# Kernel optimization log

Hardware: AMD Instinct MI355X
Metric: run time of the kernel (lower is better)

## Reference

```python
import jax, jax.numpy as jnp
import numpy as np

B, L, D, NLAYERS, KCONV = 8, 2048, 1024, 3, 4


def setup_inputs() -> dict:
    key = jax.random.key(0)
    ks = jax.random.split(key, 8)
    inp = {
        "x": jax.random.normal(ks[0], (B, L, D), jnp.float32),
        "conv_w": jax.random.normal(ks[1], (NLAYERS, D, KCONV), jnp.float32) * 0.02,
        "conv_b": jnp.zeros((NLAYERS, D), jnp.float32),
        "wr_w": jax.random.normal(ks[2], (NLAYERS, D, D), jnp.float32) * (1.0 / np.sqrt(D)),
        "wr_b": jnp.zeros((NLAYERS, D), jnp.float32),
        "wi_w": jax.random.normal(ks[3], (NLAYERS, D, D), jnp.float32) * (1.0 / np.sqrt(D)),
        "wi_b": jnp.zeros((NLAYERS, D), jnp.float32),
        "log_a": 3.0 + 0.1 * jax.random.normal(ks[4], (NLAYERS, D), jnp.float32),
        "wo_w": jax.random.normal(ks[5], (NLAYERS, D, D), jnp.float32) * (1.0 / np.sqrt(D)),
        "norm_w": jnp.ones((NLAYERS, D), jnp.float32),
        "norm_out_w": jnp.ones((D,), jnp.float32),
    }
    return inp


def _rmsnorm(x, w, eps=1e-6):
    return x * w * jax.lax.rsqrt(jnp.mean(x * x, axis=-1, keepdims=True) + eps)


def _parallel_scan(a, b):
    # h_t = a_t * h_{t-1} + b_t  via log-space prefix scan (h0 = 0)
    a32 = a.astype(jnp.float32)
    b32 = b.astype(jnp.float32)
    log_A = jnp.cumsum(jnp.log(jnp.maximum(a32, 1e-7)), axis=1)
    log_A = jnp.maximum(log_A, -80.0)  # a<=1 so log_A<=0 already
    A = jnp.exp(log_A)
    h = A * jnp.cumsum(b32 * jnp.exp(-log_A), axis=1)
    return h.astype(a.dtype)


def _rglru_layer(x, cw, cb, wrw, wrb, wiw, wib, la, wow, nw):
    # causal depthwise conv1d, kernel 4, left pad 3
    Lx = x.shape[1]
    xp = jnp.pad(x, ((0, 0), (KCONV - 1, 0), (0, 0)))
    x_conv = cb + sum(xp[:, k:k + Lx, :] * cw[:, k] for k in range(KCONV))
    r_t = jax.nn.sigmoid(x_conv @ wrw.T + wrb)
    i_t = jax.nn.sigmoid(x_conv @ wiw.T + wib)
    a_base = jax.nn.sigmoid(la.astype(jnp.float32)).astype(x.dtype)
    a_t = a_base ** (8.0 * r_t)
    b_t = jnp.sqrt(jnp.clip(1.0 - a_t * a_t, 1e-6, None)) * (i_t * x_conv)
    h = _parallel_scan(a_t, b_t)
    return _rmsnorm(h @ wow.T, nw)


def reference(x, conv_w, conv_b, wr_w, wr_b, wi_w, wi_b, log_a, wo_w, norm_w, norm_out_w):
    h = x
    for l in range(NLAYERS):
        h = _rglru_layer(h, conv_w[l], conv_b[l], wr_w[l], wr_b[l],
                         wi_w[l], wi_b[l], log_a[l], wo_w[l], norm_w[l])
    return _rmsnorm(h, norm_out_w)
```

## Files before the change

### kernel.cpp

```cpp
#include <hip/hip_runtime.h>
#include <type_traits>

#define BDIM 8
#define LDIM 2048
#define DDIM 1024
#define NL 3
#define K4 4
#define MDIM (BDIM * LDIM)
#define BK32 32
#define NT32 (DDIM / BK32)

typedef __bf16 bf16x8 __attribute__((ext_vector_type(8)));
typedef __bf16 bf16x4 __attribute__((ext_vector_type(4)));
typedef float f32x4 __attribute__((ext_vector_type(4)));
typedef const __attribute__((address_space(1))) void gvoid_t;
typedef __attribute__((address_space(3))) void svoid_t;

__device__ __forceinline__ void load16(const void* g, void* lds_uniform) {
    __builtin_amdgcn_global_load_lds((gvoid_t*)g, (svoid_t*)lds_uniform, 16, 0, 0);
}

#define SBAR()                                  \
    do {                                        \
        asm volatile("" ::: "memory");          \
        __builtin_amdgcn_s_barrier();           \
        asm volatile("" ::: "memory");          \
    } while (0)
#define WAITV(N) asm volatile("s_waitcnt vmcnt(" #N ")" ::: "memory")

__global__ void cvt_bf16(const float* __restrict__ s, __bf16* __restrict__ d, int n) {
    int i = blockIdx.x * 256 + threadIdx.x;
    if (i < n) d[i] = (__bf16)s[i];
}

__global__ __launch_bounds__(256) void cvt_interleave(const float* __restrict__ wr,
                                                      const float* __restrict__ wi,
                                                      __bf16* __restrict__ w2, int n) {
    int i = blockIdx.x * 256 + threadIdx.x;
    if (i >= n) return;
    int k = i & (DDIM - 1);
    int ld = i >> 10;
    int l = ld >> 10;
    int d = ld & (DDIM - 1);
    size_t base = ((size_t)l * 2 * DDIM + 2 * d) * DDIM + k;
    w2[base] = (__bf16)wr[i];
    w2[base + DDIM] = (__bf16)wi[i];
}

template <typename T>
__global__ __launch_bounds__(256) void conv_kernel(const T* __restrict__ X,
                                                   const float* __restrict__ cw,
                                                   const float* __restrict__ cb,
                                                   __bf16* __restrict__ XC) {
    int idx = blockIdx.x * 256 + threadIdx.x;
    int d = (idx & (DDIM / 4 - 1)) << 2;
    int t = (idx >> 8) & (LDIM - 1);
    int b = idx >> 19;
    float wv[4][4];
    *(float4*)wv[0] = ((const float4*)cw)[d + 0];
    *(float4*)wv[1] = ((const float4*)cw)[d + 1];
    *(float4*)wv[2] = ((const float4*)cw)[d + 2];
    *(float4*)wv[3] = ((const float4*)cw)[d + 3];
    float4 cbv = *(const float4*)(cb + d);
    float acc[4] = {cbv.x, cbv.y, cbv.z, cbv.w};
#pragma unroll
    for (int k = 0; k < K4; k++) {
        int tt = t + k - (K4 - 1);
        if (tt >= 0) {
            size_t off = ((size_t)(b * LDIM + tt) << 10) + d;
            float xv[4];
            if constexpr (std::is_same<T, float>::value) {
                float4 v = *(const float4*)(X + off);
                xv[0] = v.x; xv[1] = v.y; xv[2] = v.z; xv[3] = v.w;
            } else {
                bf16x4 v = *(const bf16x4*)(X + off);
                xv[0] = (float)v.x; xv[1] = (float)v.y; xv[2] = (float)v.z; xv[3] = (float)v.w;
            }
#pragma unroll
            for (int j = 0; j < 4; j++) acc[j] += xv[j] * wv[j][k];
        }
    }
    bf16x4 o;
    o.x = (__bf16)acc[0]; o.y = (__bf16)acc[1]; o.z = (__bf16)acc[2]; o.w = (__bf16)acc[3];
    *(bf16x4*)(XC + ((size_t)(b * LDIM + t) << 10) + d) = o;
}

__global__ __launch_bounds__(512, 2) void gate_gemm(
    const __bf16* __restrict__ A, const __bf16* __restrict__ W2,
    const float* __restrict__ wrb, const float* __restrict__ wib,
    const float* __restrict__ la,
    __bf16* __restrict__ LOGA, __bf16* __restrict__ BB) {
    __shared__ __attribute__((aligned(16))) __bf16 sm[4][2][8192];
    int tid = threadIdx.x;
    int wave = tid >> 6, lane = tid & 63;
    int wm = wave >> 2, wn = wave & 3;
    int fr = lane & 15, quad = lane >> 4;

    int nx = gridDim.x;
    int bid = blockIdx.y * nx + blockIdx.x;
    int cpx = (nx * gridDim.y) >> 3;
    int sw = (bid & 7) * cpx + (bid >> 3);
    int bm0 = (sw / nx) * 256;
    int bn0 = (sw % nx) * 256;

    const __bf16* Ag = A + (size_t)bm0 * DDIM;
    const __bf16* Bg = W2 + (size_t)bn0 * DDIM;

    f32x4 acc[8][4];
    f32x4 zero = {0.f, 0.f, 0.f, 0.f};
#pragma unroll
    for (int i = 0; i < 8; i++)
#pragma unroll
        for (int j = 0; j < 4; j++) acc[i][j] = zero;

    auto STAGE = [&](int buf, int ko) {
#pragma unroll
        for (int j = 0; j < 2; j++) {
            int ci = j * 512 + tid;
            int r = ci >> 2;
            int g = (ci & 3) ^ ((r >> 1) & 3);
            size_t go = (size_t)r * DDIM + ko + g * 8;
            int lb = j * 4096 + wave * 512;
            load16(Ag + go, &sm[buf][0][lb]);
            load16(Bg + go, &sm[buf][1][lb]);
        }
    };

    STAGE(0, 0);
    STAGE(1, BK32);
    STAGE(2, 2 * BK32);
    for (int t4 = 0; t4 < NT32; t4 += 4) {
#pragma unroll
        for (int tt = 0; tt < 4; tt++) {
            int t = t4 + tt;
            if (t + 2 < NT32) { WAITV(8); }
            else if (t + 1 < NT32) { WAITV(4); }
            else { WAITV(0); }
            SBAR();
            if (t + 3 < NT32) STAGE((tt + 3) & 3, (t + 3) * BK32);
            const __bf16* Ac = &sm[tt][0][0];
            const __bf16* Bc = &sm[tt][1][0];
            bf16x8 bfm[4];
#pragma unroll
            for (int ni = 0; ni < 4; ni++) {
                int row = wn * 64 + ni * 16 + fr;
                bfm[ni] = *(const bf16x8*)(Bc + row * 32 + ((quad ^ ((row >> 1) & 3)) << 3));
            }
#pragma unroll
            for (int mh = 0; mh < 2; mh++) {
                bf16x8 af[4];
#pragma unroll
                for (int mi = 0; mi < 4; mi++) {
                    int row = wm * 128 + (mh * 4 + mi) * 16 + fr;
                    af[mi] = *(const bf16x8*)(Ac + row * 32 + ((quad ^ ((row >> 1) & 3)) << 3));
                }
                __builtin_amdgcn_s_setprio(1);
#pragma unroll
                for (int ni = 0; ni < 4; ni++)
#pragma unroll
                    for (int mi = 0; mi < 4; mi++)
                        acc[mh * 4 + mi][ni] = __builtin_amdgcn_mfma_f32_16x16x32_bf16(
                            af[mi], bfm[ni], acc[mh * 4 + mi][ni], 0, 0, 0);
                __builtin_amdgcn_s_setprio(0);
            }
        }
    }

    float* Lt = (float*)&sm[0][0][0];
    int colg = (tid & 31) * 8;
    int d0 = (bn0 >> 1) + (colg >> 1);
    float rb[4], ibv[4], lnab[4];
    {
        float4 r4 = *(const float4*)(wrb + d0);
        float4 i4 = *(const float4*)(wib + d0);
        float4 l4 = *(const float4*)(la + d0);
        float lav[4] = {l4.x, l4.y, l4.z, l4.w};
        rb[0] = r4.x; rb[1] = r4.y; rb[2] = r4.z; rb[3] = r4.w;
        ibv[0] = i4.x; ibv[1] = i4.y; ibv[2] = i4.z; ibv[3] = i4.w;
#pragma unroll
        for (int j = 0; j < 4; j++) lnab[j] = __logf(1.f / (1.f + __expf(-lav[j])));
    }
#pragma unroll
    for (int mi = 0; mi < 8; mi++) {
        __syncthreads();
#pragma unroll
        for (int ni = 0; ni < 4; ni++) {
            int col = wn * 64 + ni * 16 + fr;
#pragma unroll
            for (int reg = 0; reg < 4; reg++)
                Lt[(wm * 16 + quad * 4 + reg) * 260 + col] = acc[mi][ni][reg];
        }
        __syncthreads();
#pragma unroll
        for (int hf = 0; hf < 2; hf++) {
            int r = (tid >> 5) + hf * 16;
            int m = bm0 + (r >> 4) * 128 + mi * 16 + (r & 15);
            float vv[8];
            *(f32x4*)&vv[0] = *(const f32x4*)&Lt[r * 260 + colg];
            *(f32x4*)&vv[4] = *(const f32x4*)&Lt[r * 260 + colg + 4];
            bf16x4 xcv = *(const bf16x4*)(A + (size_t)m * DDIM + d0);
            bf16x4 og, ob;
#pragma unroll
            for (int j = 0; j < 4; j++) {
                float rv = 1.f / (1.f + __expf(-(vv[2 * j] + rb[j])));
                float iv = 1.f / (1.f + __expf(-(vv[2 * j + 1] + ibv[j])));
                float lga = 8.f * rv * lnab[j];
                float a = __expf(lga);
                float bt = sqrtf(fmaxf(1.f - a * a, 1e-6f)) * (iv * (float)xcv[j]);
                og[j] = (__bf16)lga;
                ob[j] = (__bf16)bt;
            }
            *(bf16x4*)(LOGA + (size_t)m * DDIM + d0) = og;
            *(bf16x4*)(BB + (size_t)m * DDIM + d0) = ob;
        }
    }
}

__global__ __launch_bounds__(512, 2) void out_gemm(
    const __bf16* __restrict__ A, const __bf16* __restrict__ Wo, __bf16* __restrict__ HW) {
    __shared__ __attribute__((aligned(16))) __bf16 sm[4][2][8192];
    int tid = threadIdx.x;
    int wave = tid >> 6, lane = tid & 63;
    int wm = wave >> 2, wn = wave & 3;
    int fr = lane & 15, quad = lane >> 4;

    int nx = gridDim.x;
    int bid = blockIdx.y * nx + blockIdx.x;
    int cpx = (nx * gridDim.y) >> 3;
    int sw = (bid & 7) * cpx + (bid >> 3);
    int bm0 = (sw / nx) * 256;
    int bn0 = (sw % nx) * 256;

    const __bf16* Ag = A + (size_t)bm0 * DDIM;
    const __bf16* Bg = Wo + (size_t)bn0 * DDIM;

    f32x4 acc[8][4];
    f32x4 zero = {0.f, 0.f, 0.f, 0.f};
#pragma unroll
    for (int i = 0; i < 8; i++)
#pragma unroll
        for (int j = 0; j < 4; j++) acc[i][j] = zero;

    auto STAGE = [&](int buf, int ko) {
#pragma unroll
        for (int j = 0; j < 2; j++) {
            int ci = j * 512 + tid;
            int r = ci >> 2;
            int g = (ci & 3) ^ ((r >> 1) & 3);
            size_t go = (size_t)r * DDIM + ko + g * 8;
            int lb = j * 4096 + wave * 512;
            load16(Ag + go, &sm[buf][0][lb]);
            load16(Bg + go, &sm[buf][1][lb]);
        }
    };

    STAGE(0, 0);
    STAGE(1, BK32);
    STAGE(2, 2 * BK32);
    for (int t4 = 0; t4 < NT32; t4 += 4) {
#pragma unroll
        for (int tt = 0; tt < 4; tt++) {
            int t = t4 + tt;
            if (t + 2 < NT32) { WAITV(8); }
            else if (t + 1 < NT32) { WAITV(4); }
            else { WAITV(0); }
            SBAR();
            if (t + 3 < NT32) STAGE((tt + 3) & 3, (t + 3) * BK32);
            const __bf16* Ac = &sm[tt][0][0];
            const __bf16* Bc = &sm[tt][1][0];
            bf16x8 bfm[4];
#pragma unroll
            for (int ni = 0; ni < 4; ni++) {
                int row = wn * 64 + ni * 16 + fr;
                bfm[ni] = *(const bf16x8*)(Bc + row * 32 + ((quad ^ ((row >> 1) & 3)) << 3));
            }
#pragma unroll
            for (int mh = 0; mh < 2; mh++) {
                bf16x8 af[4];
#pragma unroll
                for (int mi = 0; mi < 4; mi++) {
                    int row = wm * 128 + (mh * 4 + mi) * 16 + fr;
                    af[mi] = *(const bf16x8*)(Ac + row * 32 + ((quad ^ ((row >> 1) & 3)) << 3));
                }
                __builtin_amdgcn_s_setprio(1);
#pragma unroll
                for (int ni = 0; ni < 4; ni++)
#pragma unroll
                    for (int mi = 0; mi < 4; mi++)
                        acc[mh * 4 + mi][ni] = __builtin_amdgcn_mfma_f32_16x16x32_bf16(
                            af[mi], bfm[ni], acc[mh * 4 + mi][ni], 0, 0, 0);
                __builtin_amdgcn_s_setprio(0);
            }
        }
    }

    float* Lt = (float*)&sm[0][0][0];
    int colg = (tid & 31) * 8;
    int n0 = bn0 + colg;
#pragma unroll
    for (int mi = 0; mi < 8; mi++) {
        __syncthreads();
#pragma unroll
        for (int ni = 0; ni < 4; ni++) {
            int col = wn * 64 + ni * 16 + fr;
#pragma unroll
            for (int reg = 0; reg < 4; reg++)
                Lt[(wm * 16 + quad * 4 + reg) * 260 + col] = acc[mi][ni][reg];
        }
        __syncthreads();
#pragma unroll
        for (int hf = 0; hf < 2; hf++) {
            int r = (tid >> 5) + hf * 16;
            int m = bm0 + (r >> 4) * 128 + mi * 16 + (r & 15);
            float vv[8];
            *(f32x4*)&vv[0] = *(const f32x4*)&Lt[r * 260 + colg];
            *(f32x4*)&vv[4] = *(const f32x4*)&Lt[r * 260 + colg + 4];
            bf16x8 o;
#pragma unroll
            for (int j = 0; j < 8; j++) o[j] = (__bf16)vv[j];
            *(bf16x8*)(HW + (size_t)m * DDIM + n0) = o;
        }
    }
}

#define SC_T (LDIM / 8)
__global__ __launch_bounds__(256) void scan_kernel(const __bf16* __restrict__ LOGA,
                                                   const __bf16* __restrict__ BB,
                                                   __bf16* __restrict__ H) {
    int b = blockIdx.y;
    int dl = threadIdx.x & 31;
    int d = blockIdx.x * 32 + dl;
    int c = threadIdx.x >> 5;
    size_t base = ((size_t)b * LDIM + (size_t)c * SC_T) * DDIM + d;
    const __bf16* pga = LOGA + base;
    const __bf16* pbb = BB + base;
    __bf16* pH = H + base;

    float S = 0.f;
#pragma unroll 8
    for (int t = 0; t < SC_T; t++) S += (float)pga[(size_t)t * DDIM];
    __shared__ float sS[8][32];
    sS[c][dl] = S;
    __syncthreads();
    float L0 = 0.f;
    for (int cc = 0; cc < c; cc++) L0 += sS[cc][dl];

    float Lr = L0, lcp = fmaxf(L0, -80.f), hB = 0.f;
#pragma unroll 4
    for (int t = 0; t < SC_T; t++) {
        float lga = (float)pga[(size_t)t * DDIM];
        Lr += lga;
        float lc = fmaxf(Lr, -80.f);
        hB = __expf(lc - lcp) * hB + (float)pbb[(size_t)t * DDIM];
        lcp = lc;
    }
    float Ac = __expf(fmaxf(Lr, -80.f) - fmaxf(L0, -80.f));
    __shared__ float sA[8][32], sB[8][32];
    sA[c][dl] = Ac;
    sB[c][dl] = hB;
    __syncthreads();
    float hin = 0.f;
    for (int cc = 0; cc < c; cc++) hin = sA[cc][dl] * hin + sB[cc][dl];

    Lr = L0;
    lcp = fmaxf(L0, -80.f);
    float h = hin;
#pragma unroll 4
    for (int t = 0; t < SC_T; t++) {
        float lga = (float)pga[(size_t)t * DDIM];
        Lr += lga;
        float lc = fmaxf(Lr, -80.f);
        h = __expf(lc - lcp) * h + (float)pbb[(size_t)t * DDIM];
        lcp = lc;
        pH[(size_t)t * DDIM] = (__bf16)h;
    }
}

template <typename TI, typename TO>
__global__ __launch_bounds__(256) void rmsnorm_kernel(const TI* __restrict__ X,
                                                      const float* __restrict__ w,
                                                      TO* __restrict__ Y) {
    int row = blockIdx.x;
    int tid = threadIdx.x;
    size_t off = (size_t)row * DDIM + tid * 4;
    float v[4];
    if constexpr (std::is_same<TI, float>::value) {
        float4 t = *(const float4*)(X + off);
        v[0] = t.x; v[1] = t.y; v[2] = t.z; v[3] = t.w;
    } else {
        bf16x4 t = *(const bf16x4*)(X + off);
        v[0] = (float)t.x; v[1] = (float)t.y; v[2] = (float)t.z; v[3] = (float)t.w;
    }
    float s = v[0] * v[0] + v[1] * v[1] + v[2] * v[2] + v[3] * v[3];
#pragma unroll
    for (int o = 32; o > 0; o >>= 1) s += __shfl_down(s, o);
    __shared__ float sw[4];
    if ((tid & 63) == 0) sw[tid >> 6] = s;
    __syncthreads();
    float tot = sw[0] + sw[1] + sw[2] + sw[3];
    float scale = rsqrtf(tot * (1.f / (float)DDIM) + 1e-6f);
    float4 wv = ((const float4*)w)[tid];
    float o0 = v[0] * wv.x * scale, o1 = v[1] * wv.y * scale;
    float o2 = v[2] * wv.z * scale, o3 = v[3] * wv.w * scale;
    if constexpr (std::is_same<TO, float>::value) {
        float4 o = {o0, o1, o2, o3};
        *(float4*)(Y + off) = o;
    } else {
        bf16x4 o;
        o.x = (__bf16)o0; o.y = (__bf16)o1; o.z = (__bf16)o2; o.w = (__bf16)o3;
        *(bf16x4*)(Y + off) = o;
    }
}

extern "C" void kernel_launch(void* const* d_in, const int* in_sizes, int n_in,
                              void* d_out, int out_size, void* d_ws, size_t ws_size,
                              hipStream_t stream) {
    const float* x = (const float*)d_in[0];
    const float* conv_w = (const float*)d_in[1];
    const float* conv_b = (const float*)d_in[2];
    const float* wr_w = (const float*)d_in[3];
    const float* wr_b = (const float*)d_in[4];
    const float* wi_w = (const float*)d_in[5];
    const float* wi_b = (const float*)d_in[6];
    const float* log_a = (const float*)d_in[7];
    const float* wo_w = (const float*)d_in[8];
    const float* norm_w = (const float*)d_in[9];
    const float* norm_out_w = (const float*)d_in[10];

    const size_t W2SZ = (size_t)NL * 2 * DDIM * DDIM;
    const size_t WOSZ = (size_t)NL * DDIM * DDIM;
    const size_t MD = (size_t)MDIM * DDIM;
    __bf16* w2 = (__bf16*)d_ws;
    __bf16* wo16 = w2 + W2SZ;
    __bf16* XC = wo16 + WOSZ;
    __bf16* LGA = XC + MD;
    __bf16* BBf = LGA + MD;
    __bf16* Hb = BBf + MD;
    __bf16* HWb = Hb + MD;
    __bf16* PNb = HWb + MD;

    int nw = (int)WOSZ;
    cvt_interleave<<<(nw + 255) / 256, 256, 0, stream>>>(wr_w, wi_w, w2, nw);
    cvt_bf16<<<(nw + 255) / 256, 256, 0, stream>>>(wo_w, wo16, nw);

    for (int l = 0; l < NL; l++) {
        if (l == 0)
            conv_kernel<float><<<(MDIM * (DDIM / 4)) / 256, 256, 0, stream>>>(
                x, conv_w, conv_b, XC);
        else
            conv_kernel<__bf16><<<(MDIM * (DDIM / 4)) / 256, 256, 0, stream>>>(
                PNb, conv_w + (size_t)l * DDIM * K4, conv_b + (size_t)l * DDIM, XC);
        gate_gemm<<<dim3(2 * DDIM / 256, MDIM / 256), 512, 0, stream>>>(
            XC, w2 + (size_t)l * 2 * DDIM * DDIM,
            wr_b + (size_t)l * DDIM, wi_b + (size_t)l * DDIM, log_a + (size_t)l * DDIM,
            LGA, BBf);
        scan_kernel<<<dim3(DDIM / 32, BDIM), 256, 0, stream>>>(LGA, BBf, Hb);
        out_gemm<<<dim3(DDIM / 256, MDIM / 256), 512, 0, stream>>>(
            Hb, wo16 + (size_t)l * DDIM * DDIM, HWb);
        rmsnorm_kernel<__bf16, __bf16><<<MDIM, 256, 0, stream>>>(
            HWb, norm_w + (size_t)l * DDIM, PNb);
    }
    rmsnorm_kernel<__bf16, float><<<MDIM, 256, 0, stream>>>(PNb, norm_out_w, (float*)d_out);
}
```

Measured before the change: 1.004 ms.

## Shrink GEMM tiles to 128x128 single-buffered, widen scan chunks, fuse final norms

Both GEMMs go from 256x256 tiles with 512 threads and a 4-stage async LDS pipeline to 128x128 tiles with 256 threads, BK=64 and one LDS buffer with a barrier before and after each load. The scan kernel splits the sequence into 32 chunks per block (1024 threads) instead of 8, for more parallelism. The last layer's rmsnorm and the output rmsnorm are fused into one kernel, saving a launch and one pass over memory. Smaller tiles add occupancy and grid size, but they lower per-tile reuse and drop the load/compute overlap, which may hurt GEMM throughput.

Result: faster. 891.3 us (-11.3%).

```diff
diff --git a/kernel.cpp b/kernel.cpp
--- a/kernel.cpp
+++ b/kernel.cpp
@@ -7,8 +7,6 @@
 #define NL 3
 #define K4 4
 #define MDIM (BDIM * LDIM)
-#define BK32 32
-#define NT32 (DDIM / BK32)
 
 typedef __bf16 bf16x8 __attribute__((ext_vector_type(8)));
 typedef __bf16 bf16x4 __attribute__((ext_vector_type(4)));
@@ -19,14 +17,6 @@
 __device__ __forceinline__ void load16(const void* g, void* lds_uniform) {
     __builtin_amdgcn_global_load_lds((gvoid_t*)g, (svoid_t*)lds_uniform, 16, 0, 0);
 }
-
-#define SBAR()                                  \
-    do {                                        \
-        asm volatile("" ::: "memory");          \
-        __builtin_amdgcn_s_barrier();           \
-        asm volatile("" ::: "memory");          \
-    } while (0)
-#define WAITV(N) asm volatile("s_waitcnt vmcnt(" #N ")" ::: "memory")
 
 __global__ void cvt_bf16(const float* __restrict__ s, __bf16* __restrict__ d, int n) {
     int i = blockIdx.x * 256 + threadIdx.x;
@@ -85,89 +75,80 @@
     *(bf16x4*)(XC + ((size_t)(b * LDIM + t) << 10) + d) = o;
 }
 
-__global__ __launch_bounds__(512, 2) void gate_gemm(
+__global__ __launch_bounds__(256, 3) void gate_gemm(
     const __bf16* __restrict__ A, const __bf16* __restrict__ W2,
     const float* __restrict__ wrb, const float* __restrict__ wib,
     const float* __restrict__ la,
     __bf16* __restrict__ LOGA, __bf16* __restrict__ BB) {
-    __shared__ __attribute__((aligned(16))) __bf16 sm[4][2][8192];
+    __shared__ __attribute__((aligned(16))) __bf16 sm[16384];
     int tid = threadIdx.x;
     int wave = tid >> 6, lane = tid & 63;
-    int wm = wave >> 2, wn = wave & 3;
+    int wm = wave >> 1, wn = wave & 1;
     int fr = lane & 15, quad = lane >> 4;
 
     int nx = gridDim.x;
     int bid = blockIdx.y * nx + blockIdx.x;
     int cpx = (nx * gridDim.y) >> 3;
     int sw = (bid & 7) * cpx + (bid >> 3);
-    int bm0 = (sw / nx) * 256;
-    int bn0 = (sw % nx) * 256;
+    int bm0 = (sw / nx) * 128;
+    int bn0 = (sw % nx) * 128;
 
     const __bf16* Ag = A + (size_t)bm0 * DDIM;
     const __bf16* Bg = W2 + (size_t)bn0 * DDIM;
 
-    f32x4 acc[8][4];
+    f32x4 acc[4][4];
     f32x4 zero = {0.f, 0.f, 0.f, 0.f};
 #pragma unroll
-    for (int i = 0; i < 8; i++)
+    for (int i = 0; i < 4; i++)
 #pragma unroll
         for (int j = 0; j < 4; j++) acc[i][j] = zero;
 
-    auto STAGE = [&](int buf, int ko) {
-#pragma unroll
-        for (int j = 0; j < 2; j++) {
-            int ci = j * 512 + tid;
-            int r = ci >> 2;
-            int g = (ci & 3) ^ ((r >> 1) & 3);
-            size_t go = (size_t)r * DDIM + ko + g * 8;
-            int lb = j * 4096 + wave * 512;
-            load16(Ag + go, &sm[buf][0][lb]);
-            load16(Bg + go, &sm[buf][1][lb]);
-        }
-    };
-
-    STAGE(0, 0);
-    STAGE(1, BK32);
-    STAGE(2, 2 * BK32);
-    for (int t4 = 0; t4 < NT32; t4 += 4) {
-#pragma unroll
-        for (int tt = 0; tt < 4; tt++) {
-            int t = t4 + tt;
-            if (t + 2 < NT32) { WAITV(8); }
-            else if (t + 1 < NT32) { WAITV(4); }
-            else { WAITV(0); }
-            SBAR();
-            if (t + 3 < NT32) STAGE((tt + 3) & 3, (t + 3) * BK32);
-            const __bf16* Ac = &sm[tt][0][0];
-            const __bf16* Bc = &sm[tt][1][0];
-            bf16x8 bfm[4];
+    const __bf16* gAs[4];
+    const __bf16* gBs[4];
+    int ub[4];
+#pragma unroll
+    for (int j = 0; j < 4; j++) {
+        int ci = j * 256 + tid;
+        int r = ci >> 3, sc = ci & 7;
+        int g = sc ^ (r & 7);
+        gAs[j] = Ag + (size_t)r * DDIM + g * 8;
+        gBs[j] = Bg + (size_t)r * DDIM + g * 8;
+        ub[j] = (j * 256 + wave * 64) * 8;
+    }
+
+    for (int ko = 0; ko < DDIM; ko += 64) {
+        if (ko) __syncthreads();
+#pragma unroll
+        for (int j = 0; j < 4; j++) {
+            load16(gAs[j] + ko, sm + ub[j]);
+            load16(gBs[j] + ko, sm + 8192 + ub[j]);
+        }
+        __syncthreads();
+#pragma unroll
+        for (int kw = 0; kw < 2; kw++) {
+            bf16x8 af[4], bf[4];
+#pragma unroll
+            for (int mi = 0; mi < 4; mi++) {
+                int row = wm * 64 + mi * 16 + fr;
+                af[mi] = *(const bf16x8*)(sm + row * 64 + (((kw * 4 + quad) ^ (row & 7)) << 3));
+            }
 #pragma unroll
             for (int ni = 0; ni < 4; ni++) {
                 int row = wn * 64 + ni * 16 + fr;
-                bfm[ni] = *(const bf16x8*)(Bc + row * 32 + ((quad ^ ((row >> 1) & 3)) << 3));
-            }
-#pragma unroll
-            for (int mh = 0; mh < 2; mh++) {
-                bf16x8 af[4];
-#pragma unroll
-                for (int mi = 0; mi < 4; mi++) {
-                    int row = wm * 128 + (mh * 4 + mi) * 16 + fr;
-                    af[mi] = *(const bf16x8*)(Ac + row * 32 + ((quad ^ ((row >> 1) & 3)) << 3));
-                }
-                __builtin_amdgcn_s_setprio(1);
-#pragma unroll
-                for (int ni = 0; ni < 4; ni++)
-#pragma unroll
-                    for (int mi = 0; mi < 4; mi++)
-                        acc[mh * 4 + mi][ni] = __builtin_amdgcn_mfma_f32_16x16x32_bf16(
-                            af[mi], bfm[ni], acc[mh * 4 + mi][ni], 0, 0, 0);
-                __builtin_amdgcn_s_setprio(0);
-            }
-        }
-    }
-
-    float* Lt = (float*)&sm[0][0][0];
-    int colg = (tid & 31) * 8;
+                bf[ni] = *(const bf16x8*)(sm + 8192 + row * 64 + (((kw * 4 + quad) ^ (row & 7)) << 3));
+            }
+#pragma unroll
+            for (int ni = 0; ni < 4; ni++)
+#pragma unroll
+                for (int mi = 0; mi < 4; mi++)
+                    acc[mi][ni] = __builtin_amdgcn_mfma_f32_16x16x32_bf16(
+                        af[mi], bf[ni], acc[mi][ni], 0, 0, 0);
+        }
+    }
+
+    float* Lt = (float*)&sm[0];
+    int wrow = (wave >> 1) * 16, wcol = (wave & 1) * 64;
+    int colg = (tid & 15) * 8;
     int d0 = (bn0 >> 1) + (colg >> 1);
     float rb[4], ibv[4], lnab[4];
     {
@@ -181,23 +162,23 @@
         for (int j = 0; j < 4; j++) lnab[j] = __logf(1.f / (1.f + __expf(-lav[j])));
     }
 #pragma unroll
-    for (int mi = 0; mi < 8; mi++) {
+    for (int mi = 0; mi < 4; mi++) {
         __syncthreads();
 #pragma unroll
         for (int ni = 0; ni < 4; ni++) {
-            int col = wn * 64 + ni * 16 + fr;
+            int col = wcol + ni * 16 + fr;
 #pragma unroll
             for (int reg = 0; reg < 4; reg++)
-                Lt[(wm * 16 + quad * 4 + reg) * 260 + col] = acc[mi][ni][reg];
+                Lt[(wrow + quad * 4 + reg) * 132 + col] = acc[mi][ni][reg];
         }
         __syncthreads();
 #pragma unroll
         for (int hf = 0; hf < 2; hf++) {
-            int r = (tid >> 5) + hf * 16;
-            int m = bm0 + (r >> 4) * 128 + mi * 16 + (r & 15);
+            int lrow = (tid >> 4) + hf * 16;
+            int m = bm0 + (lrow >> 4) * 64 + mi * 16 + (lrow & 15);
             float vv[8];
-            *(f32x4*)&vv[0] = *(const f32x4*)&Lt[r * 260 + colg];
-            *(f32x4*)&vv[4] = *(const f32x4*)&Lt[r * 260 + colg + 4];
+            *(f32x4*)&vv[0] = *(const f32x4*)&Lt[lrow * 132 + colg];
+            *(f32x4*)&vv[4] = *(const f32x4*)&Lt[lrow * 132 + colg + 4];
             bf16x4 xcv = *(const bf16x4*)(A + (size_t)m * DDIM + d0);
             bf16x4 og, ob;
 #pragma unroll
@@ -216,105 +197,96 @@
     }
 }
 
-__global__ __launch_bounds__(512, 2) void out_gemm(
+__global__ __launch_bounds__(256, 3) void out_gemm(
     const __bf16* __restrict__ A, const __bf16* __restrict__ Wo, __bf16* __restrict__ HW) {
-    __shared__ __attribute__((aligned(16))) __bf16 sm[4][2][8192];
+    __shared__ __attribute__((aligned(16))) __bf16 sm[16384];
     int tid = threadIdx.x;
     int wave = tid >> 6, lane = tid & 63;
-    int wm = wave >> 2, wn = wave & 3;
+    int wm = wave >> 1, wn = wave & 1;
     int fr = lane & 15, quad = lane >> 4;
 
     int nx = gridDim.x;
     int bid = blockIdx.y * nx + blockIdx.x;
     int cpx = (nx * gridDim.y) >> 3;
     int sw = (bid & 7) * cpx + (bid >> 3);
-    int bm0 = (sw / nx) * 256;
-    int bn0 = (sw % nx) * 256;
+    int bm0 = (sw / nx) * 128;
+    int bn0 = (sw % nx) * 128;
 
     const __bf16* Ag = A + (size_t)bm0 * DDIM;
     const __bf16* Bg = Wo + (size_t)bn0 * DDIM;
 
-    f32x4 acc[8][4];
+    f32x4 acc[4][4];
     f32x4 zero = {0.f, 0.f, 0.f, 0.f};
 #pragma unroll
-    for (int i = 0; i < 8; i++)
+    for (int i = 0; i < 4; i++)
 #pragma unroll
         for (int j = 0; j < 4; j++) acc[i][j] = zero;
 
-    auto STAGE = [&](int buf, int ko) {
-#pragma unroll
-        for (int j = 0; j < 2; j++) {
-            int ci = j * 512 + tid;
-            int r = ci >> 2;
-            int g = (ci & 3) ^ ((r >> 1) & 3);
-            size_t go = (size_t)r * DDIM + ko + g * 8;
-            int lb = j * 4096 + wave * 512;
-            load16(Ag + go, &sm[buf][0][lb]);
-            load16(Bg + go, &sm[buf][1][lb]);
-        }
-    };
-
-    STAGE(0, 0);
-    STAGE(1, BK32);
-    STAGE(2, 2 * BK32);
-    for (int t4 = 0; t4 < NT32; t4 += 4) {
-#pragma unroll
-        for (int tt = 0; tt < 4; tt++) {
-            int t = t4 + tt;
-            if (t + 2 < NT32) { WAITV(8); }
-            else if (t + 1 < NT32) { WAITV(4); }
-            else { WAITV(0); }
-            SBAR();
-            if (t + 3 < NT32) STAGE((tt + 3) & 3, (t + 3) * BK32);
-            const __bf16* Ac = &sm[tt][0][0];
-            const __bf16* Bc = &sm[tt][1][0];
-            bf16x8 bfm[4];
+    const __bf16* gAs[4];
+    const __bf16* gBs[4];
+    int ub[4];
+#pragma unroll
+    for (int j = 0; j < 4; j++) {
+        int ci = j * 256 + tid;
+        int r = ci >> 3, sc = ci & 7;
+        int g = sc ^ (r & 7);
+        gAs[j] = Ag + (size_t)r * DDIM + g * 8;
+        gBs[j] = Bg + (size_t)r * DDIM + g * 8;
+        ub[j] = (j * 256 + wave * 64) * 8;
+    }
+
+    for (int ko = 0; ko < DDIM; ko += 64) {
+        if (ko) __syncthreads();
+#pragma unroll
+        for (int j = 0; j < 4; j++) {
+            load16(gAs[j] + ko, sm + ub[j]);
+            load16(gBs[j] + ko, sm + 8192 + ub[j]);
+        }
+        __syncthreads();
+#pragma unroll
+        for (int kw = 0; kw < 2; kw++) {
+            bf16x8 af[4], bf[4];
+#pragma unroll
+            for (int mi = 0; mi < 4; mi++) {
+                int row = wm * 64 + mi * 16 + fr;
+                af[mi] = *(const bf16x8*)(sm + row * 64 + (((kw * 4 + quad) ^ (row & 7)) << 3));
+            }
 #pragma unroll
             for (int ni = 0; ni < 4; ni++) {
                 int row = wn * 64 + ni * 16 + fr;
-                bfm[ni] = *(const bf16x8*)(Bc + row * 32 + ((quad ^ ((row >> 1) & 3)) << 3));
-            }
-#pragma unroll
-            for (int mh = 0; mh < 2; mh++) {
-                bf16x8 af[4];
-#pragma unroll
-                for (int mi = 0; mi < 4; mi++) {
-                    int row = wm * 128 + (mh * 4 + mi) * 16 + fr;
-                    af[mi] = *(const bf16x8*)(Ac + row * 32 + ((quad ^ ((row >> 1) & 3)) << 3));
-                }
-                __builtin_amdgcn_s_setprio(1);
-#pragma unroll
-                for (int ni = 0; ni < 4; ni++)
-#pragma unroll
-                    for (int mi = 0; mi < 4; mi++)
-                        acc[mh * 4 + mi][ni] = __builtin_amdgcn_mfma_f32_16x16x32_bf16(
-                            af[mi], bfm[ni], acc[mh * 4 + mi][ni], 0, 0, 0);
-                __builtin_amdgcn_s_setprio(0);
-            }
-        }
-    }
-
-    float* Lt = (float*)&sm[0][0][0];
-    int colg = (tid & 31) * 8;
+                bf[ni] = *(const bf16x8*)(sm + 8192 + row * 64 + (((kw * 4 + quad) ^ (row & 7)) << 3));
+            }
+#pragma unroll
+            for (int ni = 0; ni < 4; ni++)
+#pragma unroll
+                for (int mi = 0; mi < 4; mi++)
+                    acc[mi][ni] = __builtin_amdgcn_mfma_f32_16x16x32_bf16(
+                        af[mi], bf[ni], acc[mi][ni], 0, 0, 0);
+        }
+    }
+
+    float* Lt = (float*)&sm[0];
+    int wrow = (wave >> 1) * 16, wcol = (wave & 1) * 64;
+    int colg = (tid & 15) * 8;
     int n0 = bn0 + colg;
 #pragma unroll
-    for (int mi = 0; mi < 8; mi++) {
+    for (int mi = 0; mi < 4; mi++) {
         __syncthreads();
 #pragma unroll
         for (int ni = 0; ni < 4; ni++) {
-            int col = wn * 64 + ni * 16 + fr;
+            int col = wcol + ni * 16 + fr;
 #pragma unroll
             for (int reg = 0; reg < 4; reg++)
-                Lt[(wm * 16 + quad * 4 + reg) * 260 + col] = acc[mi][ni][reg];
+                Lt[(wrow + quad * 4 + reg) * 132 + col] = acc[mi][ni][reg];
         }
         __syncthreads();
 #pragma unroll
         for (int hf = 0; hf < 2; hf++) {
-            int r = (tid >> 5) + hf * 16;
-            int m = bm0 + (r >> 4) * 128 + mi * 16 + (r & 15);
+            int lrow = (tid >> 4) + hf * 16;
+            int m = bm0 + (lrow >> 4) * 64 + mi * 16 + (lrow & 15);
             float vv[8];
-            *(f32x4*)&vv[0] = *(const f32x4*)&Lt[r * 260 + colg];
-            *(f32x4*)&vv[4] = *(const f32x4*)&Lt[r * 260 + colg + 4];
+            *(f32x4*)&vv[0] = *(const f32x4*)&Lt[lrow * 132 + colg];
+            *(f32x4*)&vv[4] = *(const f32x4*)&Lt[lrow * 132 + colg + 4];
             bf16x8 o;
 #pragma unroll
             for (int j = 0; j < 8; j++) o[j] = (__bf16)vv[j];
@@ -323,23 +295,24 @@
     }
 }
 
-#define SC_T (LDIM / 8)
-__global__ __launch_bounds__(256) void scan_kernel(const __bf16* __restrict__ LOGA,
-                                                   const __bf16* __restrict__ BB,
-                                                   __bf16* __restrict__ H) {
+#define SCH 32
+#define SCT 64
+__global__ __launch_bounds__(1024) void scan_kernel(const __bf16* __restrict__ LOGA,
+                                                    const __bf16* __restrict__ BB,
+                                                    __bf16* __restrict__ H) {
     int b = blockIdx.y;
     int dl = threadIdx.x & 31;
     int d = blockIdx.x * 32 + dl;
     int c = threadIdx.x >> 5;
-    size_t base = ((size_t)b * LDIM + (size_t)c * SC_T) * DDIM + d;
+    size_t base = ((size_t)b * LDIM + (size_t)c * SCT) * DDIM + d;
     const __bf16* pga = LOGA + base;
     const __bf16* pbb = BB + base;
     __bf16* pH = H + base;
 
     float S = 0.f;
 #pragma unroll 8
-    for (int t = 0; t < SC_T; t++) S += (float)pga[(size_t)t * DDIM];
-    __shared__ float sS[8][32];
+    for (int t = 0; t < SCT; t++) S += (float)pga[(size_t)t * DDIM];
+    __shared__ float sS[SCH][32];
     sS[c][dl] = S;
     __syncthreads();
     float L0 = 0.f;
@@ -347,7 +320,7 @@
 
     float Lr = L0, lcp = fmaxf(L0, -80.f), hB = 0.f;
 #pragma unroll 4
-    for (int t = 0; t < SC_T; t++) {
+    for (int t = 0; t < SCT; t++) {
         float lga = (float)pga[(size_t)t * DDIM];
         Lr += lga;
         float lc = fmaxf(Lr, -80.f);
@@ -355,7 +328,7 @@
         lcp = lc;
     }
     float Ac = __expf(fmaxf(Lr, -80.f) - fmaxf(L0, -80.f));
-    __shared__ float sA[8][32], sB[8][32];
+    __shared__ float sA[SCH][32], sB[SCH][32];
     sA[c][dl] = Ac;
     sB[c][dl] = hB;
     __syncthreads();
@@ -366,7 +339,7 @@
     lcp = fmaxf(L0, -80.f);
     float h = hin;
 #pragma unroll 4
-    for (int t = 0; t < SC_T; t++) {
+    for (int t = 0; t < SCT; t++) {
         float lga = (float)pga[(size_t)t * DDIM];
         Lr += lga;
         float lc = fmaxf(Lr, -80.f);
@@ -412,6 +385,38 @@
     }
 }
 
+__global__ __launch_bounds__(256) void rmsnorm2_kernel(const __bf16* __restrict__ X,
+                                                       const float* __restrict__ w1,
+                                                       const float* __restrict__ w2,
+                                                       float* __restrict__ Y) {
+    int row = blockIdx.x;
+    int tid = threadIdx.x;
+    size_t off = (size_t)row * DDIM + tid * 4;
+    bf16x4 t = *(const bf16x4*)(X + off);
+    float v[4] = {(float)t.x, (float)t.y, (float)t.z, (float)t.w};
+    float s = v[0] * v[0] + v[1] * v[1] + v[2] * v[2] + v[3] * v[3];
+#pragma unroll
+    for (int o = 32; o > 0; o >>= 1) s += __shfl_down(s, o);
+    __shared__ float sw[8];
+    if ((tid & 63) == 0) sw[tid >> 6] = s;
+    __syncthreads();
+    float scale1 = rsqrtf((sw[0] + sw[1] + sw[2] + sw[3]) * (1.f / (float)DDIM) + 1e-6f);
+    float4 w1v = ((const float4*)w1)[tid];
+    float y[4] = {v[0] * w1v.x * scale1, v[1] * w1v.y * scale1,
+                  v[2] * w1v.z * scale1, v[3] * w1v.w * scale1};
+    float s2 = y[0] * y[0] + y[1] * y[1] + y[2] * y[2] + y[3] * y[3];
+#pragma unroll
+    for (int o = 32; o > 0; o >>= 1) s2 += __shfl_down(s2, o);
+    __syncthreads();
+    if ((tid & 63) == 0) sw[4 + (tid >> 6)] = s2;
+    __syncthreads();
+    float scale2 = rsqrtf((sw[4] + sw[5] + sw[6] + sw[7]) * (1.f / (float)DDIM) + 1e-6f);
+    float4 w2v = ((const float4*)w2)[tid];
+    float4 o = {y[0] * w2v.x * scale2, y[1] * w2v.y * scale2,
+                y[2] * w2v.z * scale2, y[3] * w2v.w * scale2};
+    *(float4*)(Y + off) = o;
+}
+
 extern "C" void kernel_launch(void* const* d_in, const int* in_sizes, int n_in,
                               void* d_out, int out_size, void* d_ws, size_t ws_size,
                               hipStream_t stream) {
@@ -450,15 +455,17 @@
         else
             conv_kernel<__bf16><<<(MDIM * (DDIM / 4)) / 256, 256, 0, stream>>>(
                 PNb, conv_w + (size_t)l * DDIM * K4, conv_b + (size_t)l * DDIM, XC);
-        gate_gemm<<<dim3(2 * DDIM / 256, MDIM / 256), 512, 0, stream>>>(
+        gate_gemm<<<dim3(2 * DDIM / 128, MDIM / 128), 256, 0, stream>>>(
             XC, w2 + (size_t)l * 2 * DDIM * DDIM,
             wr_b + (size_t)l * DDIM, wi_b + (size_t)l * DDIM, log_a + (size_t)l * DDIM,
             LGA, BBf);
-        scan_kernel<<<dim3(DDIM / 32, BDIM), 256, 0, stream>>>(LGA, BBf, Hb);
-        out_gemm<<<dim3(DDIM / 256, MDIM / 256), 512, 0, stream>>>(
+        scan_kernel<<<dim3(DDIM / 32, BDIM), 1024, 0, stream>>>(LGA, BBf, Hb);
+        out_gemm<<<dim3(DDIM / 128, MDIM / 128), 256, 0, stream>>>(
             Hb, wo16 + (size_t)l * DDIM * DDIM, HWb);
-        rmsnorm_kernel<__bf16, __bf16><<<MDIM, 256, 0, stream>>>(
-            HWb, norm_w + (size_t)l * DDIM, PNb);
-    }
-    rmsnorm_kernel<__bf16, float><<<MDIM, 256, 0, stream>>>(PNb, norm_out_w, (float*)d_out);
-}
+        if (l < NL - 1)
+            rmsnorm_kernel<__bf16, __bf16><<<MDIM, 256, 0, stream>>>(
+                HWb, norm_w + (size_t)l * DDIM, PNb);
+    }
+    rmsnorm2_kernel<<<MDIM, 256, 0, stream>>>(
+        HWb, norm_w + (size_t)(NL - 1) * DDIM, norm_out_w, (float*)d_out);
+}
```
